# Kernel tuning notes

Measured on AMD Instinct MI355X. Metric: run time of the kernel, lower is better.

Reference implementation:

```python
import jax, jax.numpy as jnp
import numpy as np

B, S, D, H = 2, 2048, 2048, 16
HD = D // H  # 128


def setup_inputs() -> dict:
    key = jax.random.key(0)
    ks = jax.random.split(key, 5)
    scale = 0.02
    return {
        "hidden_states": jax.random.normal(ks[0], (B, S, D), dtype=jnp.float32),
        "Wqkv_w": jax.random.normal(ks[1], (3 * D, D), dtype=jnp.float32) * scale,
        "Wqkv_b": jax.random.normal(ks[2], (3 * D,), dtype=jnp.float32) * scale,
        "out_w": jax.random.normal(ks[3], (D, D), dtype=jnp.float32) * scale,
        "out_b": jax.random.normal(ks[4], (D,), dtype=jnp.float32) * scale,
    }


def reference(hidden_states, Wqkv_w, Wqkv_b, out_w, out_b):
    b, s, d = hidden_states.shape
    # QKV projection (torch Linear: x @ W.T + b)
    qkv = hidden_states @ Wqkv_w.T + Wqkv_b          # [b, s, 3d]
    qkv = qkv.reshape(b, s, 3, H, HD)                 # 'b s (three h d)'
    q, k, v = qkv[:, :, 0], qkv[:, :, 1], qkv[:, :, 2]  # [b, s, h, hd]
    softmax_scale = 1.0 / np.float32(np.sqrt(HD))
    # full quadratic scores, matching the naive baddbmm path
    scores = jnp.einsum('bthd,bshd->bhts', q, k) * softmax_scale  # [b,h,t,s]
    # causal=False (module default), dropout_p=0.0 -> no mask, no dropout
    attn = jax.nn.softmax(scores, axis=-1)
    ctx = jnp.einsum('bhts,bshd->bthd', attn, v)      # [b, t, h, hd]
    ctx = ctx.reshape(b, s, d)
    return ctx @ out_w.T + out_b
```

## Files before the change

### kernel.cpp

```cpp
#include <hip/hip_runtime.h>
#include <cstdint>
#include <cstddef>

#define B_ 2
#define S_ 2048
#define D_ 2048
#define H_ 16
#define HD_ 128
#define NTOK 4096
#define NQKV 6144

typedef unsigned short u16;
typedef __attribute__((ext_vector_type(8))) __bf16 bf16x8;
typedef __attribute__((ext_vector_type(4))) float f32x4;

__device__ __forceinline__ u16 f2bf(float f) {
  uint32_t u = __builtin_bit_cast(uint32_t, f);
  u = (u + 0x7FFFu + ((u >> 16) & 1u)) >> 16;
  return (u16)u;
}

__device__ __forceinline__ void gload_lds16(const void* g, void* l) {
  __builtin_amdgcn_global_load_lds(
      (const __attribute__((address_space(1))) void*)g,
      (__attribute__((address_space(3))) void*)l, 16, 0, 0);
}

__global__ void cvt_all(const float* __restrict__ hs, const float* __restrict__ wqkv,
                        const float* __restrict__ wo,
                        u16* __restrict__ hsb, u16* __restrict__ wqkvb,
                        u16* __restrict__ wob) {
  const int n1 = (B_ * S_ * D_) / 8;
  const int n2 = n1 + (NQKV * D_) / 8;
  const int n3 = n2 + (D_ * D_) / 8;
  int idx = blockIdx.x * blockDim.x + threadIdx.x;
  int stride = gridDim.x * blockDim.x;
  for (int i = idx; i < n3; i += stride) {
    const float* src; u16* dst; int j;
    if (i < n1)      { src = hs;   dst = hsb;   j = i; }
    else if (i < n2) { src = wqkv; dst = wqkvb; j = i - n1; }
    else             { src = wo;   dst = wob;   j = i - n2; }
    const float4* s = (const float4*)(src + (size_t)j * 8);
    float4 a = s[0], b = s[1];
    union { u16 u[8]; uint4 v; } o;
    o.u[0] = f2bf(a.x); o.u[1] = f2bf(a.y); o.u[2] = f2bf(a.z); o.u[3] = f2bf(a.w);
    o.u[4] = f2bf(b.x); o.u[5] = f2bf(b.y); o.u[6] = f2bf(b.z); o.u[7] = f2bf(b.w);
    *(uint4*)(dst + (size_t)j * 8) = o.v;
  }
}


#define PH_MID() do { asm volatile("s_barrier" ::: "memory"); \
  __builtin_amdgcn_s_setprio(1); } while (0)
#define PH_END() do { __builtin_amdgcn_s_setprio(0); \
  asm volatile("s_barrier" ::: "memory"); } while (0)
#define PH_END_VM(n) do { __builtin_amdgcn_s_setprio(0); \
  asm volatile("s_waitcnt vmcnt(" #n ")" ::: "memory"); \
  asm volatile("s_barrier" ::: "memory"); } while (0)

#define STA(sl,buf,ko) gload_lds16(aSrc + (size_t)(sl)*64*D_ + (ko), aDst + (buf)*8192  + (sl)*4096)
#define STB(sl,buf,ko) gload_lds16(bSrc + (size_t)(sl)*64*D_ + (ko), bDst + (buf)*12288 + (sl)*4096)

#define LOADB(buf) do { _Pragma("unroll") for (int nf = 0; nf < 3; ++nf) \
  _Pragma("unroll") for (int kk = 0; kk < 2; ++kk) \
    breg[nf][kk] = *(const bf16x8*)(sB + (buf)*12288 + (wn*48 + nf*16 + fr)*64 + ((((kk<<2)|fq)^swz)<<3)); } while (0)
#define LOADA_A(buf,q) do { _Pragma("unroll") for (int mm = 0; mm < 2; ++mm) \
  _Pragma("unroll") for (int kk = 0; kk < 2; ++kk) \
    arA[mm][kk] = *(const bf16x8*)(sA + (buf)*8192 + (wm*64 + ((q)*2+mm)*16 + fr)*64 + ((((kk<<2)|fq)^swz)<<3)); } while (0)
#define LOADA_B(buf,q) do { _Pragma("unroll") for (int mm = 0; mm < 2; ++mm) \
  _Pragma("unroll") for (int kk = 0; kk < 2; ++kk) \
    arB[mm][kk] = *(const bf16x8*)(sA + (buf)*8192 + (wm*64 + ((q)*2+mm)*16 + fr)*64 + ((((kk<<2)|fq)^swz)<<3)); } while (0)
#define MFMA12_A(q) do { _Pragma("unroll") for (int kk = 0; kk < 2; ++kk) \
  _Pragma("unroll") for (int mm = 0; mm < 2; ++mm) \
  _Pragma("unroll") for (int nf = 0; nf < 3; ++nf) \
    acc[(q)*2+mm][nf] = __builtin_amdgcn_mfma_f32_16x16x32_bf16(arA[mm][kk], breg[nf][kk], acc[(q)*2+mm][nf], 0, 0, 0); } while (0)
#define MFMA12_B(q) do { _Pragma("unroll") for (int kk = 0; kk < 2; ++kk) \
  _Pragma("unroll") for (int mm = 0; mm < 2; ++mm) \
  _Pragma("unroll") for (int nf = 0; nf < 3; ++nf) \
    acc[(q)*2+mm][nf] = __builtin_amdgcn_mfma_f32_16x16x32_bf16(arB[mm][kk], breg[nf][kk], acc[(q)*2+mm][nf], 0, 0, 0); } while (0)

__global__ __launch_bounds__(512, 4) void qkv_gemm(
    const u16* __restrict__ hsb, const u16* __restrict__ wb,
    const float* __restrict__ bias,
    u16* __restrict__ qb, u16* __restrict__ kb, u16* __restrict__ vT)
{
  __shared__ alignas(1024) u16 sA[2 * 8192];
  __shared__ alignas(1024) u16 sB[2 * 12288];
  const int tid = threadIdx.x;
  const int lane = tid & 63, wid = tid >> 6;
  const int wm = wid >> 2, wn = wid & 3;
  const int fr = lane & 15, fq = lane >> 4;
  const int swz = fr & 7;
  const int m0 = blockIdx.x * 128, n0 = blockIdx.y * 192;

  const int r8 = tid >> 3, g8 = (tid & 7) ^ (r8 & 7);
  const u16* aSrc = hsb + (size_t)(m0 + r8) * D_ + g8 * 8;
  const u16* bSrc = wb  + (size_t)(n0 + r8) * D_ + g8 * 8;
  u16* aDst = sA + wid * 512;
  u16* bDst = sB + wid * 512;

  f32x4 acc[4][3];
  f32x4 z = {0.f, 0.f, 0.f, 0.f};
#pragma unroll
  for (int m = 0; m < 4; ++m)
#pragma unroll
    for (int n = 0; n < 3; ++n) acc[m][n] = z;

  bf16x8 breg[3][2], arA[2][2], arB[2][2];

  STB(0,0,0); STB(1,0,0); STB(2,0,0); STA(0,0,0); STA(1,0,0);
  STB(0,1,64); STB(1,1,64); STB(2,1,64);
  asm volatile("s_waitcnt vmcnt(3)" ::: "memory");
  asm volatile("s_barrier" ::: "memory");

#pragma unroll 1
  for (int j = 0; j < 15; ++j) {
    const int kA1 = (2*j + 1) * 64;
    const int kB2 = (2*j + 2) * 64;
    const int kB3 = (2*j + 3) * 64;
    LOADB(0); LOADA_A(0,0); LOADA_B(0,1); STA(0,1,kA1); STA(1,1,kA1);
      PH_MID(); MFMA12_A(0); PH_END();
    STB(0,0,kB2); STB(1,0,kB2); STB(2,0,kB2);
      PH_MID(); MFMA12_B(1); PH_END_VM(3);
    LOADB(1); LOADA_A(1,0); LOADA_B(1,1); STA(0,0,kB2); STA(1,0,kB2);
      PH_MID(); MFMA12_A(0); PH_END();
    STB(0,1,kB3); STB(1,1,kB3); STB(2,1,kB3);
      PH_MID(); MFMA12_B(1); PH_END_VM(3);
  }
  {
    const int kA31 = 31 * 64;
    LOADB(0); LOADA_A(0,0); LOADA_B(0,1); STA(0,1,kA31); STA(1,1,kA31);
      PH_MID(); MFMA12_A(0); PH_END();
      PH_MID(); MFMA12_B(1); PH_END_VM(0);
    LOADB(1); LOADA_A(1,0); LOADA_B(1,1);
      PH_MID(); MFMA12_A(0); PH_END();
      PH_MID(); MFMA12_B(1); PH_END();
  }

  const float qscale = 0.08838834764831845f;
#pragma unroll
  for (int mf = 0; mf < 4; ++mf)
#pragma unroll
    for (int nf = 0; nf < 3; ++nf) {
      int col = n0 + wn * 48 + nf * 16 + fr;
      float bv = bias[col];
      int t = col >> 11;
      int d2 = col & 2047;
      int h = d2 >> 7, hd = d2 & 127;
#pragma unroll
      for (int r = 0; r < 4; ++r) {
        int row = m0 + wm * 64 + mf * 16 + fq * 4 + r;
        int bb = row >> 11, s = row & 2047;
        int bh = bb * H_ + h;
        float val = acc[mf][nf][r] + bv;
        if (t == 0)      qb[((size_t)bh * S_ + s) * HD_ + hd] = f2bf(val * qscale);
        else if (t == 1) kb[((size_t)bh * S_ + s) * HD_ + hd] = f2bf(val);
        else             vT[((size_t)bh * HD_ + hd) * S_ + s] = f2bf(val);
      }
    }
}

__device__ __forceinline__ void gemm_bt_tile(
    const u16* __restrict__ A, const u16* __restrict__ B,
    int lda, int ldb, int K, int m0, int n0,
    u16* As, u16* Bs, f32x4 acc[4][4])
{
  const int tid = threadIdx.x;
  const int lane = tid & 63;
  const int wid = tid >> 6;
  const int wr = wid >> 1, wc = wid & 1;
  const int fr = lane & 15, fq = lane >> 4;

  for (int k0 = 0; k0 < K; k0 += 32) {
    __syncthreads();
#pragma unroll
    for (int i = 0; i < 2; ++i) {
      int cbase = (i * 4 + wid) * 64;
      int c = cbase + lane;
      int r = c >> 2, c8 = (c & 3) * 8;
      gload_lds16(A + (size_t)(m0 + r) * lda + k0 + c8, As + (size_t)cbase * 8);
      gload_lds16(B + (size_t)(n0 + r) * ldb + k0 + c8, Bs + (size_t)cbase * 8);
    }
    __syncthreads();

    bf16x8 a[4], b[4];
#pragma unroll
    for (int m = 0; m < 4; ++m)
      a[m] = *(const bf16x8*)&As[(wr * 64 + m * 16 + fr) * 32 + fq * 8];
#pragma unroll
    for (int n = 0; n < 4; ++n)
      b[n] = *(const bf16x8*)&Bs[(wc * 64 + n * 16 + fr) * 32 + fq * 8];
#pragma unroll
    for (int m = 0; m < 4; ++m)
#pragma unroll
      for (int n = 0; n < 4; ++n)
        acc[m][n] = __builtin_amdgcn_mfma_f32_16x16x32_bf16(a[m], b[n], acc[m][n], 0, 0, 0);
  }
}

__global__ __launch_bounds__(256) void out_gemm(
    const u16* __restrict__ ctx, const u16* __restrict__ wo,
    const float* __restrict__ bias, float* __restrict__ out)
{
  __shared__ alignas(16) u16 As[128 * 32];
  __shared__ alignas(16) u16 Bs[128 * 32];
  f32x4 acc[4][4];
  f32x4 z = {0.f, 0.f, 0.f, 0.f};
#pragma unroll
  for (int m = 0; m < 4; ++m)
#pragma unroll
    for (int n = 0; n < 4; ++n) acc[m][n] = z;

  int m0 = blockIdx.x * 128, n0 = blockIdx.y * 128;
  gemm_bt_tile(ctx, wo, D_, D_, D_, m0, n0, As, Bs, acc);

  const int lane = threadIdx.x & 63;
  const int wid = threadIdx.x >> 6;
  const int wr = wid >> 1, wc = wid & 1;
  const int fr = lane & 15, fq = lane >> 4;
#pragma unroll
  for (int m = 0; m < 4; ++m)
#pragma unroll
    for (int n = 0; n < 4; ++n) {
      int col = n0 + wc * 64 + n * 16 + fr;
      float bv = bias[col];
#pragma unroll
      for (int r = 0; r < 4; ++r) {
        int row = m0 + wr * 64 + m * 16 + fq * 4 + r;
        out[(size_t)row * D_ + col] = acc[m][n][r] + bv;
      }
    }
}

#define STAGEKV(kvv, buf) do { _Pragma("unroll") \
  for (int i = 0; i < 4; ++i) { \
    int lk = i * 256 + tid; int rk = lk >> 4, sk = lk & 15; \
    gload_lds16(Kg + (size_t)((kvv) + rk) * HD_ + ((sk ^ (rk & 7)) << 3), \
                &Kl[buf][i * 2048 + wid * 512]); \
    int rv = lk >> 3, sv = lk & 7; \
    gload_lds16(Vg + (size_t)rv * S_ + (kvv) + ((sv ^ (rv & 7)) << 3), \
                &Vl[buf][i * 2048 + wid * 512]); \
  } } while (0)

__global__ __launch_bounds__(256, 2) void attn(
    const u16* __restrict__ qb, const u16* __restrict__ kb,
    const u16* __restrict__ vT, u16* __restrict__ ctx)
{
  __shared__ alignas(1024) u16 Kl[2][64 * 128];
  __shared__ alignas(1024) u16 Vl[2][128 * 64];
  __shared__ alignas(16) u16 Pl[4][32 * 64];

  const int tid = threadIdx.x, lane = tid & 63, wid = tid >> 6;
  const int fr = lane & 15, fq = lane >> 4;
  const int bh = blockIdx.y;
  const int q0 = blockIdx.x * 128 + wid * 32;
  f32x4 z = {0.f, 0.f, 0.f, 0.f};

  const u16* Kg = kb + (size_t)bh * S_ * HD_;
  const u16* Vg = vT + (size_t)bh * HD_ * S_;

  STAGEKV(0, 0);

  const u16* qbase = qb + ((size_t)bh * S_ + q0) * HD_;
  bf16x8 qa[2][4];
#pragma unroll
  for (int h = 0; h < 2; ++h)
#pragma unroll
    for (int kc = 0; kc < 4; ++kc)
      qa[h][kc] = *(const bf16x8*)(qbase + (size_t)(h * 16 + fr) * HD_ + kc * 32 + fq * 8);

  f32x4 accv[2][8];
#pragma unroll
  for (int h = 0; h < 2; ++h)
#pragma unroll
    for (int n = 0; n < 8; ++n) accv[h][n] = z;
  float m_run[2] = {-1e30f, -1e30f};
  float l_run[2] = {0.f, 0.f};

  __syncthreads();
  int cur = 0;

  for (int kv = 0; kv < S_; kv += 64) {
    if (kv + 64 < S_) STAGEKV(kv + 64, cur ^ 1);

    const u16* Kc = Kl[cur];
    const u16* Vc = Vl[cur];

    f32x4 sc[2][4];
    __builtin_amdgcn_s_setprio(1);
#pragma unroll
    for (int j = 0; j < 4; ++j) {
      f32x4 s0 = z, s1 = z;
#pragma unroll
      for (int kc = 0; kc < 4; ++kc) {
        int row = j * 16 + fr;
        bf16x8 kf = *(const bf16x8*)&Kc[row * 128 + ((kc * 32 + fq * 8) ^ ((row & 7) << 3))];
        s0 = __builtin_amdgcn_mfma_f32_16x16x32_bf16(kf, qa[0][kc], s0, 0, 0, 0);
        s1 = __builtin_amdgcn_mfma_f32_16x16x32_bf16(kf, qa[1][kc], s1, 0, 0, 0);
      }
      sc[0][j] = s0; sc[1][j] = s1;
    }
    __builtin_amdgcn_s_setprio(0);

    float pmax[2];
#pragma unroll
    for (int h = 0; h < 2; ++h) {
      float mx = sc[h][0][0];
#pragma unroll
      for (int j = 0; j < 4; ++j)
#pragma unroll
        for (int r = 0; r < 4; ++r) mx = fmaxf(mx, sc[h][j][r]);
      mx = fmaxf(mx, __shfl_xor(mx, 16));
      mx = fmaxf(mx, __shfl_xor(mx, 32));
      pmax[h] = mx;
    }

    int need = (pmax[0] > m_run[0] + 8.f) || (pmax[1] > m_run[1] + 8.f);
    if (__any(need)) {
#pragma unroll
      for (int h = 0; h < 2; ++h) {
        float mn = fmaxf(m_run[h], pmax[h]);
        float corr = __expf(m_run[h] - mn);
        m_run[h] = mn;
        l_run[h] *= corr;
#pragma unroll
        for (int r = 0; r < 4; ++r) {
          float rc = __shfl(corr, (lane & 48) | (fq * 4 + r));
#pragma unroll
          for (int n = 0; n < 8; ++n) accv[h][n][r] *= rc;
        }
      }
    }

    u16* Pw = Pl[wid];
#pragma unroll
    for (int h = 0; h < 2; ++h) {
      float ls = 0.f;
#pragma unroll
      for (int j = 0; j < 4; ++j) {
        union { u16 u[4]; ushort4 v; } pk;
#pragma unroll
        for (int r = 0; r < 4; ++r) {
          float p = __expf(sc[h][j][r] - m_run[h]);
          ls += p;
          pk.u[r] = f2bf(p);
        }
        int prow = h * 16 + fr;
        *(ushort4*)&Pw[prow * 64 + ((j * 16 + fq * 4) ^ ((fr & 7) << 3))] = pk.v;
      }
      ls += __shfl_xor(ls, 16);
      ls += __shfl_xor(ls, 32);
      l_run[h] += ls;
    }

    __builtin_amdgcn_s_setprio(1);
#pragma unroll
    for (int kc = 0; kc < 2; ++kc) {
      int pcol = (kc * 32 + fq * 8) ^ ((fr & 7) << 3);
      bf16x8 pa0 = *(const bf16x8*)&Pw[fr * 64 + pcol];
      bf16x8 pa1 = *(const bf16x8*)&Pw[(16 + fr) * 64 + pcol];
#pragma unroll
      for (int n = 0; n < 8; ++n) {
        int row = n * 16 + fr;
        bf16x8 vf = *(const bf16x8*)&Vc[row * 64 + ((kc * 32 + fq * 8) ^ ((row & 7) << 3))];
        accv[0][n] = __builtin_amdgcn_mfma_f32_16x16x32_bf16(pa0, vf, accv[0][n], 0, 0, 0);
        accv[1][n] = __builtin_amdgcn_mfma_f32_16x16x32_bf16(pa1, vf, accv[1][n], 0, 0, 0);
      }
    }
    __builtin_amdgcn_s_setprio(0);

    __syncthreads();
    cur ^= 1;
  }

  float inv[2][4];
#pragma unroll
  for (int h = 0; h < 2; ++h)
#pragma unroll
    for (int r = 0; r < 4; ++r) {
      float l = __shfl(l_run[h], (lane & 48) | (fq * 4 + r));
      inv[h][r] = 1.f / l;
    }
  u16* cb = ctx + (((size_t)(bh >> 4)) * S_ + q0) * D_ + (size_t)(bh & 15) * HD_;
#pragma unroll
  for (int h = 0; h < 2; ++h)
#pragma unroll
    for (int n = 0; n < 8; ++n)
#pragma unroll
      for (int r = 0; r < 4; ++r) {
        int q = h * 16 + fq * 4 + r;
        cb[(size_t)q * D_ + n * 16 + fr] = f2bf(accv[h][n][r] * inv[h][r]);
      }
}

extern "C" void kernel_launch(void* const* d_in, const int* in_sizes, int n_in,
                              void* d_out, int out_size, void* d_ws, size_t ws_size,
                              hipStream_t stream) {
  const float* hs   = (const float*)d_in[0];
  const float* wqkv = (const float*)d_in[1];
  const float* bqkv = (const float*)d_in[2];
  const float* wo   = (const float*)d_in[3];
  const float* bo   = (const float*)d_in[4];
  float* out = (float*)d_out;

  char* ws = (char*)d_ws;
  u16* hsb   = (u16*)(ws);
  u16* wqkvb = (u16*)(ws + 16777216);
  u16* wob   = (u16*)(ws + 41943040);
  u16* qb    = (u16*)(ws + 50331648);
  u16* kb    = (u16*)(ws + 67108864);
  u16* vT    = (u16*)(ws + 83886080);
  u16* ctx   = (u16*)(ws + 100663296);

  cvt_all<<<2048, 256, 0, stream>>>(hs, wqkv, wo, hsb, wqkvb, wob);

  qkv_gemm<<<dim3(NTOK / 128, NQKV / 192), 512, 0, stream>>>(hsb, wqkvb, bqkv, qb, kb, vT);
  attn<<<dim3(S_ / 128, B_ * H_), 256, 0, stream>>>(qb, kb, vT, ctx);
  out_gemm<<<dim3(NTOK / 128, D_ / 128), 256, 0, stream>>>(ctx, wob, bo, out);
}
```

Measured before the change: 297.1 us.

## Rewrite output projection GEMM with double-buffered swizzled LDS pipeline and 8 waves

Replaces the simple single-buffered output GEMM (two syncthreads per K=32 step, unswizzled LDS) with a version of the qkv_gemm's ping-pong schedule. It uses K=64 tiles, double-buffered XOR-swizzled LDS, direct global-to-LDS loads interleaved with MFMA phases under s_setprio, and 512 threads per block. The aim is to hide global load latency, reduce LDS bank conflicts and barrier overhead, and raise MFMA utilisation. In exchange the kernel uses more LDS per block and a hand-tuned vmcnt schedule that must match the issue order.

```diff
diff --git a/kernel.cpp b/kernel.cpp
--- a/kernel.cpp
+++ b/kernel.cpp
@@ -49,7 +49,6 @@
   }
 }
 
-
 #define PH_MID() do { asm volatile("s_barrier" ::: "memory"); \
   __builtin_amdgcn_s_setprio(1); } while (0)
 #define PH_END() do { __builtin_amdgcn_s_setprio(0); \
@@ -57,6 +56,7 @@
 #define PH_END_VM(n) do { __builtin_amdgcn_s_setprio(0); \
   asm volatile("s_waitcnt vmcnt(" #n ")" ::: "memory"); \
   asm volatile("s_barrier" ::: "memory"); } while (0)
+
 
 #define STA(sl,buf,ko) gload_lds16(aSrc + (size_t)(sl)*64*D_ + (ko), aDst + (buf)*8192  + (sl)*4096)
 #define STB(sl,buf,ko) gload_lds16(bSrc + (size_t)(sl)*64*D_ + (ko), bDst + (buf)*12288 + (sl)*4096)
@@ -160,74 +160,95 @@
     }
 }
 
-__device__ __forceinline__ void gemm_bt_tile(
-    const u16* __restrict__ A, const u16* __restrict__ B,
-    int lda, int ldb, int K, int m0, int n0,
-    u16* As, u16* Bs, f32x4 acc[4][4])
-{
-  const int tid = threadIdx.x;
-  const int lane = tid & 63;
-  const int wid = tid >> 6;
-  const int wr = wid >> 1, wc = wid & 1;
-  const int fr = lane & 15, fq = lane >> 4;
-
-  for (int k0 = 0; k0 < K; k0 += 32) {
-    __syncthreads();
-#pragma unroll
-    for (int i = 0; i < 2; ++i) {
-      int cbase = (i * 4 + wid) * 64;
-      int c = cbase + lane;
-      int r = c >> 2, c8 = (c & 3) * 8;
-      gload_lds16(A + (size_t)(m0 + r) * lda + k0 + c8, As + (size_t)cbase * 8);
-      gload_lds16(B + (size_t)(n0 + r) * ldb + k0 + c8, Bs + (size_t)cbase * 8);
-    }
-    __syncthreads();
-
-    bf16x8 a[4], b[4];
-#pragma unroll
-    for (int m = 0; m < 4; ++m)
-      a[m] = *(const bf16x8*)&As[(wr * 64 + m * 16 + fr) * 32 + fq * 8];
-#pragma unroll
-    for (int n = 0; n < 4; ++n)
-      b[n] = *(const bf16x8*)&Bs[(wc * 64 + n * 16 + fr) * 32 + fq * 8];
-#pragma unroll
-    for (int m = 0; m < 4; ++m)
-#pragma unroll
-      for (int n = 0; n < 4; ++n)
-        acc[m][n] = __builtin_amdgcn_mfma_f32_16x16x32_bf16(a[m], b[n], acc[m][n], 0, 0, 0);
-  }
-}
-
-__global__ __launch_bounds__(256) void out_gemm(
+
+#define OSTA(sl,buf,ko) gload_lds16(aSrcO + (size_t)(sl)*64*D_ + (ko), aDstO + (buf)*8192 + (sl)*4096)
+#define OSTB(sl,buf,ko) gload_lds16(bSrcO + (size_t)(sl)*64*D_ + (ko), bDstO + (buf)*8192 + (sl)*4096)
+
+#define OLOADB(buf) do { _Pragma("unroll") for (int nf = 0; nf < 2; ++nf) \
+  _Pragma("unroll") for (int kk = 0; kk < 2; ++kk) \
+    obreg[nf][kk] = *(const bf16x8*)(sB + (buf)*8192 + (wn*32 + nf*16 + fr)*64 + ((((kk<<2)|fq)^swz)<<3)); } while (0)
+#define OLOADA_A(buf,q) do { _Pragma("unroll") for (int mm = 0; mm < 2; ++mm) \
+  _Pragma("unroll") for (int kk = 0; kk < 2; ++kk) \
+    oarA[mm][kk] = *(const bf16x8*)(sA + (buf)*8192 + (wm*64 + ((q)*2+mm)*16 + fr)*64 + ((((kk<<2)|fq)^swz)<<3)); } while (0)
+#define OLOADA_B(buf,q) do { _Pragma("unroll") for (int mm = 0; mm < 2; ++mm) \
+  _Pragma("unroll") for (int kk = 0; kk < 2; ++kk) \
+    oarB[mm][kk] = *(const bf16x8*)(sA + (buf)*8192 + (wm*64 + ((q)*2+mm)*16 + fr)*64 + ((((kk<<2)|fq)^swz)<<3)); } while (0)
+#define OMFMA8_A(q) do { _Pragma("unroll") for (int kk = 0; kk < 2; ++kk) \
+  _Pragma("unroll") for (int mm = 0; mm < 2; ++mm) \
+  _Pragma("unroll") for (int nf = 0; nf < 2; ++nf) \
+    acc[(q)*2+mm][nf] = __builtin_amdgcn_mfma_f32_16x16x32_bf16(oarA[mm][kk], obreg[nf][kk], acc[(q)*2+mm][nf], 0, 0, 0); } while (0)
+#define OMFMA8_B(q) do { _Pragma("unroll") for (int kk = 0; kk < 2; ++kk) \
+  _Pragma("unroll") for (int mm = 0; mm < 2; ++mm) \
+  _Pragma("unroll") for (int nf = 0; nf < 2; ++nf) \
+    acc[(q)*2+mm][nf] = __builtin_amdgcn_mfma_f32_16x16x32_bf16(oarB[mm][kk], obreg[nf][kk], acc[(q)*2+mm][nf], 0, 0, 0); } while (0)
+
+__global__ __launch_bounds__(512, 4) void out_gemm(
     const u16* __restrict__ ctx, const u16* __restrict__ wo,
     const float* __restrict__ bias, float* __restrict__ out)
 {
-  __shared__ alignas(16) u16 As[128 * 32];
-  __shared__ alignas(16) u16 Bs[128 * 32];
-  f32x4 acc[4][4];
+  __shared__ alignas(1024) u16 sA[2 * 8192];
+  __shared__ alignas(1024) u16 sB[2 * 8192];
+  const int tid = threadIdx.x;
+  const int lane = tid & 63, wid = tid >> 6;
+  const int wm = wid >> 2, wn = wid & 3;
+  const int fr = lane & 15, fq = lane >> 4;
+  const int swz = fr & 7;
+  const int m0 = blockIdx.x * 128, n0 = blockIdx.y * 128;
+
+  const int r8 = tid >> 3, g8 = (tid & 7) ^ (r8 & 7);
+  const u16* aSrcO = ctx + (size_t)(m0 + r8) * D_ + g8 * 8;
+  const u16* bSrcO = wo  + (size_t)(n0 + r8) * D_ + g8 * 8;
+  u16* aDstO = sA + wid * 512;
+  u16* bDstO = sB + wid * 512;
+
+  f32x4 acc[4][2];
   f32x4 z = {0.f, 0.f, 0.f, 0.f};
 #pragma unroll
   for (int m = 0; m < 4; ++m)
 #pragma unroll
-    for (int n = 0; n < 4; ++n) acc[m][n] = z;
-
-  int m0 = blockIdx.x * 128, n0 = blockIdx.y * 128;
-  gemm_bt_tile(ctx, wo, D_, D_, D_, m0, n0, As, Bs, acc);
-
-  const int lane = threadIdx.x & 63;
-  const int wid = threadIdx.x >> 6;
-  const int wr = wid >> 1, wc = wid & 1;
-  const int fr = lane & 15, fq = lane >> 4;
-#pragma unroll
-  for (int m = 0; m < 4; ++m)
-#pragma unroll
-    for (int n = 0; n < 4; ++n) {
-      int col = n0 + wc * 64 + n * 16 + fr;
+    for (int n = 0; n < 2; ++n) acc[m][n] = z;
+
+  bf16x8 obreg[2][2], oarA[2][2], oarB[2][2];
+
+  OSTB(0,0,0); OSTB(1,0,0); OSTA(0,0,0); OSTA(1,0,0);
+  OSTB(0,1,64); OSTB(1,1,64);
+  asm volatile("s_waitcnt vmcnt(2)" ::: "memory");
+  asm volatile("s_barrier" ::: "memory");
+
+#pragma unroll 1
+  for (int j = 0; j < 15; ++j) {
+    const int kA1 = (2*j + 1) * 64;
+    const int kB2 = (2*j + 2) * 64;
+    const int kB3 = (2*j + 3) * 64;
+    OLOADB(0); OLOADA_A(0,0); OLOADA_B(0,1); OSTA(0,1,kA1); OSTA(1,1,kA1);
+      PH_MID(); OMFMA8_A(0); PH_END();
+    OSTB(0,0,kB2); OSTB(1,0,kB2);
+      PH_MID(); OMFMA8_B(1); PH_END_VM(2);
+    OLOADB(1); OLOADA_A(1,0); OLOADA_B(1,1); OSTA(0,0,kB2); OSTA(1,0,kB2);
+      PH_MID(); OMFMA8_A(0); PH_END();
+    OSTB(0,1,kB3); OSTB(1,1,kB3);
+      PH_MID(); OMFMA8_B(1); PH_END_VM(2);
+  }
+  {
+    const int kA31 = 31 * 64;
+    OLOADB(0); OLOADA_A(0,0); OLOADA_B(0,1); OSTA(0,1,kA31); OSTA(1,1,kA31);
+      PH_MID(); OMFMA8_A(0); PH_END();
+      PH_MID(); OMFMA8_B(1); PH_END_VM(0);
+    OLOADB(1); OLOADA_A(1,0); OLOADA_B(1,1);
+      PH_MID(); OMFMA8_A(0); PH_END();
+      PH_MID(); OMFMA8_B(1); PH_END();
+  }
+
+#pragma unroll
+  for (int mf = 0; mf < 4; ++mf)
+#pragma unroll
+    for (int nf = 0; nf < 2; ++nf) {
+      int col = n0 + wn * 32 + nf * 16 + fr;
       float bv = bias[col];
 #pragma unroll
       for (int r = 0; r < 4; ++r) {
-        int row = m0 + wr * 64 + m * 16 + fq * 4 + r;
-        out[(size_t)row * D_ + col] = acc[m][n][r] + bv;
+        int row = m0 + wm * 64 + mf * 16 + fq * 4 + r;
+        out[(size_t)row * D_ + col] = acc[mf][nf][r] + bv;
       }
     }
 }
@@ -416,5 +437,5 @@
 
   qkv_gemm<<<dim3(NTOK / 128, NQKV / 192), 512, 0, stream>>>(hsb, wqkvb, bqkv, qb, kb, vT);
   attn<<<dim3(S_ / 128, B_ * H_), 256, 0, stream>>>(qb, kb, vT, ctx);
-  out_gemm<<<dim3(NTOK / 128, D_ / 128), 256, 0, stream>>>(ctx, wob, bo, out);
-}
+  out_gemm<<<dim3(NTOK / 128, D_ / 128), 512, 0, stream>>>(ctx, wob, bo, out);
+}
```

Measured after the change: 286.8 us. 3.5% less time.
